# Optimization experiments

Measured on AMD Instinct MI355X. Metric: run time of the kernel, lower is better.

## Reference

```python
import jax, jax.numpy as jnp
import numpy as np

DEPTH = 128
NEG_MAX = -jnp.finfo(jnp.float32).max


def setup_inputs() -> dict:
    key = jax.random.key(0)
    ks = jax.random.split(key, 10)
    B, S, F, C = 16, 2048, 512, 1000
    x = jax.random.normal(ks[0], (B, S, F), dtype=jnp.float32)
    attention_mask = jax.random.randint(ks[1], (B, S, S), 0, 2) == 1
    s = 1.0 / np.sqrt(F)
    Wq = jax.random.uniform(ks[2], (F, DEPTH), jnp.float32, -s, s)
    bq = jax.random.uniform(ks[3], (DEPTH,), jnp.float32, -s, s)
    Wk = jax.random.uniform(ks[4], (F, DEPTH), jnp.float32, -s, s)
    bk = jax.random.uniform(ks[5], (DEPTH,), jnp.float32, -s, s)
    Wv = jax.random.uniform(ks[6], (F, DEPTH), jnp.float32, -s, s)
    bv = jax.random.uniform(ks[7], (DEPTH,), jnp.float32, -s, s)
    sl = 1.0 / np.sqrt(DEPTH)
    Wl = jax.random.uniform(ks[8], (DEPTH, C), jnp.float32, -sl, sl)
    bl = jax.random.uniform(ks[9], (C,), jnp.float32, -sl, sl)
    return {"x": x, "attention_mask": attention_mask,
            "Wq": Wq, "bq": bq, "Wk": Wk, "bk": bk,
            "Wv": Wv, "bv": bv, "Wl": Wl, "bl": bl}


def reference(x, attention_mask, Wq, bq, Wk, bk, Wv, bv, Wl, bl):
    # x: [B, S, F]; single-head attention with depth=128
    q = (x @ Wq + bq) * (DEPTH ** -0.5)          # [B, S, D] (is_scaled_dot_product)
    k = x @ Wk + bk                               # [B, S, D]
    v = x @ Wv + bv                               # [B, S, D]
    logit = jnp.einsum('bsd,btd->bst', q, k)      # [B, S, S]
    # masked_fill_(mask, -float_max) then added to logits
    logit = logit + jnp.where(attention_mask, NEG_MAX, 0.0)
    attn = jax.nn.softmax(logit, axis=2)
    out = jnp.einsum('bst,btd->bsd', attn, v)     # [B, S, D]
    out = out @ Wl + bl                           # [B, S, C]
    return out.mean(axis=1)                       # [B, C]
```

## Files before the change

### kernel.cpp

```cpp
#include <hip/hip_runtime.h>
#include <stdint.h>

#define BB 16
#define SS 2048
#define FF 512
#define DD 128
#define CC 1000

typedef __attribute__((ext_vector_type(8))) short bf16x8;
typedef __attribute__((ext_vector_type(4))) float f32x4;

__device__ __forceinline__ unsigned short f2bf(float f) {
  unsigned x;
  __builtin_memcpy(&x, &f, 4);
  x = x + 0x7FFFu + ((x >> 16) & 1u);
  return (unsigned short)(x >> 16);
}
__device__ __forceinline__ float bf2f(unsigned short u) {
  unsigned x = ((unsigned)u) << 16;
  float f;
  __builtin_memcpy(&f, &x, 4);
  return f;
}
__device__ __forceinline__ unsigned pk2(float a, float b) {
  return (unsigned)f2bf(a) | ((unsigned)f2bf(b) << 16);
}

#define WS_WG   256
#define WS_ZG   131328
#define WS_YG   262400
#define WS_PK   270592
#define WS_Q    8659200
#define WS_K    17047808
#define WS_V    25436416
#define WS_WT   33825024
#define WS_END  34218240
#define WS_P    34218240
#define WS_END2 168435968

__global__ __launch_bounds__(256) void k_wt(const float* __restrict__ Wq,
                                            const float* __restrict__ Wk,
                                            const float* __restrict__ Wv,
                                            unsigned short* __restrict__ wt,
                                            const unsigned* __restrict__ mask,
                                            int* __restrict__ flags,
                                            float* __restrict__ wgl,
                                            float* __restrict__ zgl,
                                            float* __restrict__ ygl) {
  const int tid = threadIdx.x;
  if (blockIdx.x == 768) {
    __shared__ unsigned red;
    if (tid == 0) red = 0;
    __syncthreads();
    unsigned a = 0;
#pragma unroll
    for (int j = 0; j < 4; ++j) a |= mask[tid * 4 + j] & 0xFFFFFF00u;
    if (a) atomicOr(&red, 1u);
    __syncthreads();
    if (tid == 0) flags[0] = (red == 0) ? 1 : 0;
    for (int i = tid; i < BB * SS; i += 256) { wgl[i] = 0.f; zgl[i] = 0.f; }
    for (int i = tid; i < BB * DD; i += 256) ygl[i] = 0.f;
    return;
  }
  int idx = blockIdx.x * 256 + tid;
  int ty = idx >> 16;
  int o = idx & 65535;
  int d = o >> 9, f = o & 511;
  const float* W = ty == 0 ? Wq : (ty == 1 ? Wk : Wv);
  wt[idx] = f2bf(W[f * DD + d]);
}

__global__ __launch_bounds__(256) void k_pack(const void* __restrict__ mask,
                                              const int* __restrict__ flags,
                                              unsigned* __restrict__ pk) {
  const int tid = threadIdx.x;
  const long long base = (long long)blockIdx.x * 32768;
  const bool isInt = flags[0] != 0;
  for (int it = 0; it < 128; ++it) {
    long long e = base + it * 256 + tid;
    int val;
    if (isInt) val = ((const int*)mask)[e];
    else       val = ((const unsigned char*)mask)[e];
    unsigned long long bal = __ballot(val != 0);
    if ((tid & 31) == 0)
      pk[e >> 5] = (unsigned)((tid & 63) ? (bal >> 32) : bal);
  }
}

__global__ __launch_bounds__(256) void k_proj(const float* __restrict__ xg,
                                              const unsigned short* __restrict__ wtg,
                                              const float* __restrict__ bq,
                                              const float* __restrict__ bk,
                                              const float* __restrict__ bv,
                                              unsigned short* __restrict__ qo,
                                              unsigned short* __restrict__ ko,
                                              unsigned short* __restrict__ vo) {
  __shared__ __align__(16) char lA[8192];
  __shared__ __align__(16) char lB[8192];
  const int tid = threadIdx.x;
  const int lane = tid & 63;
  const int wv = tid >> 6;
  const int colL = lane & 15, quad = lane >> 4;
  const int blk = blockIdx.x, ty = blockIdx.y;
  const float* bias = ty == 0 ? bq : (ty == 1 ? bk : bv);
  unsigned short* outp = ty == 0 ? qo : (ty == 1 ? ko : vo);
  const float scale = ty == 0 ? 0.08838834764831845f : 1.0f;
  const unsigned short* wbase = wtg + (size_t)ty * 65536;
  const int m0 = (wv & 1) * 64, n0 = (wv >> 1) * 64;

  f32x4 acc[4][4];
  const f32x4 z4 = {0.f, 0.f, 0.f, 0.f};
#pragma unroll
  for (int mi = 0; mi < 4; ++mi)
#pragma unroll
    for (int ni = 0; ni < 4; ++ni) acc[mi][ni] = z4;

  for (int ic = 0; ic < 16; ++ic) {
    const int k0 = ic * 32;
    uint4 va[2], vb[2];
#pragma unroll
    for (int rr = 0; rr < 2; ++rr) {
      int p = rr * 256 + tid;
      int row = p >> 2, c = p & 3;
      const float* xp = xg + (size_t)(blk * 128 + row) * FF + k0 + c * 8;
      float4 x0 = *(const float4*)xp;
      float4 x1 = *(const float4*)(xp + 4);
      va[rr].x = pk2(x0.x, x0.y); va[rr].y = pk2(x0.z, x0.w);
      va[rr].z = pk2(x1.x, x1.y); va[rr].w = pk2(x1.z, x1.w);
      vb[rr] = *(const uint4*)(wbase + (size_t)row * FF + k0 + c * 8);
    }
    __syncthreads();
#pragma unroll
    for (int rr = 0; rr < 2; ++rr) {
      int p = rr * 256 + tid;
      int row = p >> 2, c = p & 3;
      int phys = c ^ ((row >> 1) & 3);
      *(uint4*)(lA + row * 64 + phys * 16) = va[rr];
      *(uint4*)(lB + row * 64 + phys * 16) = vb[rr];
    }
    __syncthreads();
    bf16x8 af[4], bfr[4];
#pragma unroll
    for (int mi = 0; mi < 4; ++mi) {
      int ar = m0 + mi * 16 + colL;
      int phys = quad ^ ((ar >> 1) & 3);
      af[mi] = *(const bf16x8*)(lA + ar * 64 + phys * 16);
    }
#pragma unroll
    for (int ni = 0; ni < 4; ++ni) {
      int br = n0 + ni * 16 + colL;
      int phys = quad ^ ((br >> 1) & 3);
      bfr[ni] = *(const bf16x8*)(lB + br * 64 + phys * 16);
    }
#pragma unroll
    for (int mi = 0; mi < 4; ++mi)
#pragma unroll
      for (int ni = 0; ni < 4; ++ni)
        acc[mi][ni] = __builtin_amdgcn_mfma_f32_16x16x32_bf16(af[mi], bfr[ni], acc[mi][ni], 0, 0, 0);
  }
#pragma unroll
  for (int ni = 0; ni < 4; ++ni) {
    int col = n0 + ni * 16 + colL;
    float bval = bias[col];
#pragma unroll
    for (int mi = 0; mi < 4; ++mi) {
#pragma unroll
      for (int r = 0; r < 4; ++r) {
        int row = blk * 128 + m0 + mi * 16 + quad * 4 + r;
        float val = (acc[mi][ni][r] + bval) * scale;
        outp[(size_t)row * DD + col] = f2bf(val);
      }
    }
  }
}

template <int MODE>
__global__ __launch_bounds__(256) void k_attn2(const unsigned short* __restrict__ qg,
                                               const unsigned short* __restrict__ kg,
                                               const unsigned* __restrict__ pk,
                                               float* __restrict__ zg,
                                               float* __restrict__ wg,
                                               unsigned short* __restrict__ pg) {
  __shared__ __align__(16) char kt[16384];
  __shared__ unsigned maskt[128 * 9];
  __shared__ float wacc[256];
  __shared__ __align__(16) unsigned short pt[128 * 64];
  const int tid = threadIdx.x;
  const int lane = tid & 63, wv = tid >> 6;
  const int colL = lane & 15, quad = lane >> 4;
  const int row0 = blockIdx.x * 128;
  const int tc = blockIdx.y;
  const int b = blockIdx.z;
  const int tbase = tc * 256;

  for (int i = tid; i < 1024; i += 256) {
    int row = i >> 3, w = i & 7;
    maskt[row * 9 + w] = pk[((size_t)b * SS + row0 + row) * 64 + tc * 8 + w];
  }
  if constexpr (MODE == 2) wacc[tid] = 0.f;

  bf16x8 qf[2][4];
#pragma unroll
  for (int mi = 0; mi < 2; ++mi) {
    int qrow = row0 + wv * 32 + mi * 16 + colL;
    const unsigned short* qp = qg + ((size_t)b * SS + qrow) * DD + quad * 8;
#pragma unroll
    for (int kk = 0; kk < 4; ++kk) qf[mi][kk] = *(const bf16x8*)(qp + kk * 32);
  }
  float z[2][4] = {{0.f, 0.f, 0.f, 0.f}, {0.f, 0.f, 0.f, 0.f}};
  float zinv[2][4];
  if constexpr (MODE == 2) {
#pragma unroll
    for (int mi = 0; mi < 2; ++mi)
#pragma unroll
      for (int r = 0; r < 4; ++r) {
        int row = row0 + wv * 32 + mi * 16 + quad * 4 + r;
        zinv[mi][r] = 1.0f / fmaxf(zg[(size_t)b * SS + row], 1e-30f);
      }
  }

  for (int kt0 = 0; kt0 < 4; ++kt0) {
    const int t0 = tbase + kt0 * 64;
    uint4 kreg[4];
#pragma unroll
    for (int rr = 0; rr < 4; ++rr) {
      int p = rr * 256 + tid;
      int row = p >> 4, c = p & 15;
      kreg[rr] = *(const uint4*)(kg + ((size_t)b * SS + t0 + row) * DD + c * 8);
    }
    __syncthreads();
#pragma unroll
    for (int rr = 0; rr < 4; ++rr) {
      int p = rr * 256 + tid;
      int row = p >> 4, c = p & 15;
      int phys = c ^ (row & 7);
      *(uint4*)(kt + row * 256 + phys * 16) = kreg[rr];
    }
    __syncthreads();
#pragma unroll
    for (int nt = 0; nt < 4; ++nt) {
      int rb = nt * 16 + colL;
      bf16x8 bb[4];
#pragma unroll
      for (int kk = 0; kk < 4; ++kk) {
        int phys = (kk * 4 + quad) ^ (rb & 7);
        bb[kk] = *(const bf16x8*)(kt + rb * 256 + phys * 16);
      }
      int tl = kt0 * 64 + nt * 16 + colL;
      int ct = nt * 16 + colL;
      int wl = tl >> 5, wb = tl & 31;
      float cs = 0.f;
#pragma unroll
      for (int mi = 0; mi < 2; ++mi) {
        f32x4 acc = {0.f, 0.f, 0.f, 0.f};
        acc = __builtin_amdgcn_mfma_f32_16x16x32_bf16(qf[mi][0], bb[0], acc, 0, 0, 0);
        acc = __builtin_amdgcn_mfma_f32_16x16x32_bf16(qf[mi][1], bb[1], acc, 0, 0, 0);
        acc = __builtin_amdgcn_mfma_f32_16x16x32_bf16(qf[mi][2], bb[2], acc, 0, 0, 0);
        acc = __builtin_amdgcn_mfma_f32_16x16x32_bf16(qf[mi][3], bb[3], acc, 0, 0, 0);
        int rbase = wv * 32 + mi * 16 + quad * 4;
#pragma unroll
        for (int r = 0; r < 4; ++r) {
          unsigned mw = maskt[(rbase + r) * 9 + wl];
          float e = ((mw >> wb) & 1u) ? 0.f : __expf(fminf(acc[r], 80.f));
          if constexpr (MODE != 2) z[mi][r] += e;
          else cs += e * zinv[mi][r];
          if constexpr (MODE == 1) {
            int rw = rbase + r;
            pt[rw * 64 + (ct ^ ((rw & 7) << 3))] = f2bf(e);
          }
        }
      }
      if constexpr (MODE == 2) {
        cs += __shfl_xor(cs, 16, 64);
        cs += __shfl_xor(cs, 32, 64);
        if (quad == 0) atomicAdd(&wacc[tl], cs);
      }
    }
    if constexpr (MODE == 1) {
      __syncthreads();
      unsigned short* prow = pg + ((size_t)b * SS + row0) * SS + t0;
#pragma unroll
      for (int i2 = 0; i2 < 4; ++i2) {
        int ii = i2 * 256 + tid;
        int rw = ii >> 3, c8 = ii & 7;
        uint4 vv = *(const uint4*)(pt + rw * 64 + ((c8 ^ (rw & 7)) * 8));
        *(uint4*)(prow + (size_t)rw * SS + c8 * 8) = vv;
      }
    }
  }
  if constexpr (MODE != 2) {
#pragma unroll
    for (int mi = 0; mi < 2; ++mi)
#pragma unroll
      for (int r = 0; r < 4; ++r) {
        float s = z[mi][r];
        s += __shfl_xor(s, 1, 64);
        s += __shfl_xor(s, 2, 64);
        s += __shfl_xor(s, 4, 64);
        s += __shfl_xor(s, 8, 64);
        if (colL == 0) {
          int row = row0 + wv * 32 + mi * 16 + quad * 4 + r;
          atomicAdd(&zg[(size_t)b * SS + row], s);
        }
      }
  } else {
    __syncthreads();
    atomicAdd(&wg[(size_t)b * SS + tbase + tid], wacc[tid]);
  }
}

__global__ __launch_bounds__(256) void k_csum(const unsigned short* __restrict__ pg,
                                              const float* __restrict__ zg,
                                              float* __restrict__ wg) {
  __shared__ float zl[256];
  const int tid = threadIdx.x;
  const int s0 = blockIdx.x * 256;
  const int b = blockIdx.y;
  zl[tid] = 1.0f / fmaxf(zg[(size_t)b * SS + s0 + tid], 1e-30f);
  __syncthreads();
  float acc[8] = {0.f, 0.f, 0.f, 0.f, 0.f, 0.f, 0.f, 0.f};
  const unsigned short* base = pg + ((size_t)b * SS + s0) * SS + tid * 8;
#pragma unroll 4
  for (int s = 0; s < 256; ++s) {
    bf16x8 pv = *(const bf16x8*)(base + (size_t)s * SS);
    float zi = zl[s];
#pragma unroll
    for (int j = 0; j < 8; ++j) acc[j] += bf2f((unsigned short)pv[j]) * zi;
  }
  float* wrow = wg + (size_t)b * SS + tid * 8;
#pragma unroll
  for (int j = 0; j < 8; ++j) atomicAdd(&wrow[j], acc[j]);
}

__global__ __launch_bounds__(256) void k_yv(const float* __restrict__ wgl,
                                            const unsigned short* __restrict__ vg,
                                            float* __restrict__ ygl) {
  const int tid = threadIdx.x;
  const int tc = blockIdx.x, b = blockIdx.y;
  const int d = tid & 127, half = tid >> 7;
  const int t0 = tc * 128 + half * 64;
  float p = 0.f;
  const float* wrow = wgl + (size_t)b * SS + t0;
  const unsigned short* vrow = vg + ((size_t)b * SS + t0) * DD + d;
#pragma unroll 8
  for (int t = 0; t < 64; ++t) p += wrow[t] * bf2f(vrow[(size_t)t * DD]);
  atomicAdd(&ygl[b * DD + d], p);
}

__global__ __launch_bounds__(256) void k_out(const float* __restrict__ ygl,
                                             const float* __restrict__ Wl,
                                             const float* __restrict__ bl,
                                             float* __restrict__ outp) {
  __shared__ float ys[DD];
  const int tid = threadIdx.x;
  const int b = blockIdx.x;
  if (tid < DD) ys[tid] = ygl[b * DD + tid] * (1.0f / 2048.0f);
  __syncthreads();
  for (int c = tid; c < CC; c += 256) {
    float a = bl[c];
#pragma unroll 16
    for (int dd = 0; dd < DD; ++dd) a += ys[dd] * Wl[dd * CC + c];
    outp[b * CC + c] = a;
  }
}

extern "C" void kernel_launch(void* const* d_in, const int* in_sizes, int n_in,
                              void* d_out, int out_size, void* d_ws, size_t ws_size,
                              hipStream_t stream) {
  const void* ptr[10];
  for (int i = 0; i < 10; ++i) ptr[i] = (i < n_in) ? d_in[i] : nullptr;
  if (n_in == 10) {
    const void *px = 0, *pm = 0, *pWl = 0, *pbl = 0;
    const void* pW[3] = {0, 0, 0};
    const void* pb[3] = {0, 0, 0};
    int nW = 0, nb = 0;
    for (int i = 0; i < 10; ++i) {
      int s = in_sizes[i];
      if (s == 16777216) px = d_in[i];
      else if (s == 67108864) pm = d_in[i];
      else if (s == 128000) pWl = d_in[i];
      else if (s == 1000) pbl = d_in[i];
      else if (s == 65536 && nW < 3) pW[nW++] = d_in[i];
      else if (s == 128 && nb < 3) pb[nb++] = d_in[i];
    }
    if (px && pm && pWl && pbl && nW == 3 && nb == 3) {
      ptr[0] = px; ptr[1] = pm;
      ptr[2] = pW[0]; ptr[3] = pb[0];
      ptr[4] = pW[1]; ptr[5] = pb[1];
      ptr[6] = pW[2]; ptr[7] = pb[2];
      ptr[8] = pWl; ptr[9] = pbl;
    }
  }
  char* ws = (char*)d_ws;
  if (ws_size < (size_t)WS_END) return;
  int* flags = (int*)ws;
  float* wg = (float*)(ws + WS_WG);
  float* zg = (float*)(ws + WS_ZG);
  float* yg = (float*)(ws + WS_YG);
  unsigned* pk = (unsigned*)(ws + WS_PK);
  unsigned short* q  = (unsigned short*)(ws + WS_Q);
  unsigned short* k  = (unsigned short*)(ws + WS_K);
  unsigned short* v  = (unsigned short*)(ws + WS_V);
  unsigned short* wt = (unsigned short*)(ws + WS_WT);
  unsigned short* pbuf = (unsigned short*)(ws + WS_P);
  const bool bigws = ws_size >= (size_t)WS_END2;

  k_wt<<<769, 256, 0, stream>>>((const float*)ptr[2], (const float*)ptr[4],
                                (const float*)ptr[6], wt,
                                (const unsigned*)ptr[1], flags, wg, zg, yg);
  k_pack<<<2048, 256, 0, stream>>>(ptr[1], flags, pk);
  k_proj<<<dim3(256, 3), 256, 0, stream>>>((const float*)ptr[0], wt,
                                           (const float*)ptr[3], (const float*)ptr[5],
                                           (const float*)ptr[7], q, k, v);
  if (bigws) {
    k_attn2<1><<<dim3(16, 8, 16), 256, 0, stream>>>(q, k, pk, zg, wg, pbuf);
    k_csum<<<dim3(8, 16), 256, 0, stream>>>(pbuf, zg, wg);
  } else {
    k_attn2<0><<<dim3(16, 8, 16), 256, 0, stream>>>(q, k, pk, zg, wg, nullptr);
    k_attn2<2><<<dim3(16, 8, 16), 256, 0, stream>>>(q, k, pk, zg, wg, nullptr);
  }
  k_yv<<<dim3(16, 16), 256, 0, stream>>>(wg, v, yg);
  k_out<<<16, 256, 0, stream>>>(yg, (const float*)ptr[8], (const float*)ptr[9],
                                (float*)d_out);
}
```

Before: 621.3 us.

## Fuse attention scores, normalization and column sums into one LDS-resident kernel

Replaces the two-pass attention (score kernel that writes unnormalized probabilities to a large global buffer, then a column-sum kernel) with one kernel. Each 512-thread block owns 32 query rows across all 2048 keys and keeps the bf16 probabilities in about 128KB of dynamic LDS. Row sums are reduced in LDS, and the normalized column sums are accumulated straight into the weight vector. K tiles are register-prefetched one chunk ahead. This removes the global P round-trip and a launch, at the cost of one block per CU from the large LDS footprint, small per-wave MFMA work between barriers, and more K reloads per batch.

```diff
diff --git a/kernel.cpp b/kernel.cpp
--- a/kernel.cpp
+++ b/kernel.cpp
@@ -35,8 +35,6 @@
 #define WS_V    25436416
 #define WS_WT   33825024
 #define WS_END  34218240
-#define WS_P    34218240
-#define WS_END2 168435968
 
 __global__ __launch_bounds__(256) void k_wt(const float* __restrict__ Wq,
                                             const float* __restrict__ Wk,
@@ -174,162 +172,119 @@
   }
 }
 
-template <int MODE>
-__global__ __launch_bounds__(256) void k_attn2(const unsigned short* __restrict__ qg,
-                                               const unsigned short* __restrict__ kg,
-                                               const unsigned* __restrict__ pk,
-                                               float* __restrict__ zg,
-                                               float* __restrict__ wg,
-                                               unsigned short* __restrict__ pg) {
-  __shared__ __align__(16) char kt[16384];
-  __shared__ unsigned maskt[128 * 9];
-  __shared__ float wacc[256];
-  __shared__ __align__(16) unsigned short pt[128 * 64];
+__global__ __launch_bounds__(512, 2) void k_fatt(const unsigned short* __restrict__ qg,
+                                                 const unsigned short* __restrict__ kg,
+                                                 const unsigned* __restrict__ pk,
+                                                 float* __restrict__ wg) {
+  extern __shared__ __align__(16) char smem[];
+  unsigned short* pt = (unsigned short*)smem;
+  char* kt = smem + 131072;
+  unsigned* mk = (unsigned*)(smem + 147456);
+  float* zfin = (float*)(smem + 155776);
+  float* zinvl = (float*)(smem + 155904);
+
   const int tid = threadIdx.x;
   const int lane = tid & 63, wv = tid >> 6;
   const int colL = lane & 15, quad = lane >> 4;
-  const int row0 = blockIdx.x * 128;
-  const int tc = blockIdx.y;
-  const int b = blockIdx.z;
-  const int tbase = tc * 256;
-
-  for (int i = tid; i < 1024; i += 256) {
-    int row = i >> 3, w = i & 7;
-    maskt[row * 9 + w] = pk[((size_t)b * SS + row0 + row) * 64 + tc * 8 + w];
-  }
-  if constexpr (MODE == 2) wacc[tid] = 0.f;
-
-  bf16x8 qf[2][4];
-#pragma unroll
-  for (int mi = 0; mi < 2; ++mi) {
-    int qrow = row0 + wv * 32 + mi * 16 + colL;
+  const int wr = wv & 1, wq = wv >> 1;
+  const int r0 = blockIdx.x * 32;
+  const int b = blockIdx.y;
+
+  for (int i = tid; i < 2048; i += 512) {
+    int row = i >> 6, w = i & 63;
+    mk[row * 65 + w] = pk[((size_t)b * SS + r0 + row) * 64 + w];
+  }
+  if (tid < 32) zfin[tid] = 0.f;
+
+  bf16x8 qf[4];
+  {
+    int qrow = r0 + wr * 16 + colL;
     const unsigned short* qp = qg + ((size_t)b * SS + qrow) * DD + quad * 8;
 #pragma unroll
-    for (int kk = 0; kk < 4; ++kk) qf[mi][kk] = *(const bf16x8*)(qp + kk * 32);
-  }
-  float z[2][4] = {{0.f, 0.f, 0.f, 0.f}, {0.f, 0.f, 0.f, 0.f}};
-  float zinv[2][4];
-  if constexpr (MODE == 2) {
-#pragma unroll
-    for (int mi = 0; mi < 2; ++mi)
-#pragma unroll
-      for (int r = 0; r < 4; ++r) {
-        int row = row0 + wv * 32 + mi * 16 + quad * 4 + r;
-        zinv[mi][r] = 1.0f / fmaxf(zg[(size_t)b * SS + row], 1e-30f);
-      }
-  }
-
-  for (int kt0 = 0; kt0 < 4; ++kt0) {
-    const int t0 = tbase + kt0 * 64;
-    uint4 kreg[4];
-#pragma unroll
-    for (int rr = 0; rr < 4; ++rr) {
-      int p = rr * 256 + tid;
-      int row = p >> 4, c = p & 15;
-      kreg[rr] = *(const uint4*)(kg + ((size_t)b * SS + t0 + row) * DD + c * 8);
-    }
-    __syncthreads();
-#pragma unroll
-    for (int rr = 0; rr < 4; ++rr) {
-      int p = rr * 256 + tid;
-      int row = p >> 4, c = p & 15;
-      int phys = c ^ (row & 7);
-      *(uint4*)(kt + row * 256 + phys * 16) = kreg[rr];
-    }
-    __syncthreads();
-#pragma unroll
-    for (int nt = 0; nt < 4; ++nt) {
-      int rb = nt * 16 + colL;
-      bf16x8 bb[4];
-#pragma unroll
-      for (int kk = 0; kk < 4; ++kk) {
-        int phys = (kk * 4 + quad) ^ (rb & 7);
-        bb[kk] = *(const bf16x8*)(kt + rb * 256 + phys * 16);
-      }
-      int tl = kt0 * 64 + nt * 16 + colL;
-      int ct = nt * 16 + colL;
-      int wl = tl >> 5, wb = tl & 31;
-      float cs = 0.f;
-#pragma unroll
-      for (int mi = 0; mi < 2; ++mi) {
-        f32x4 acc = {0.f, 0.f, 0.f, 0.f};
-        acc = __builtin_amdgcn_mfma_f32_16x16x32_bf16(qf[mi][0], bb[0], acc, 0, 0, 0);
-        acc = __builtin_amdgcn_mfma_f32_16x16x32_bf16(qf[mi][1], bb[1], acc, 0, 0, 0);
-        acc = __builtin_amdgcn_mfma_f32_16x16x32_bf16(qf[mi][2], bb[2], acc, 0, 0, 0);
-        acc = __builtin_amdgcn_mfma_f32_16x16x32_bf16(qf[mi][3], bb[3], acc, 0, 0, 0);
-        int rbase = wv * 32 + mi * 16 + quad * 4;
-#pragma unroll
-        for (int r = 0; r < 4; ++r) {
-          unsigned mw = maskt[(rbase + r) * 9 + wl];
-          float e = ((mw >> wb) & 1u) ? 0.f : __expf(fminf(acc[r], 80.f));
-          if constexpr (MODE != 2) z[mi][r] += e;
-          else cs += e * zinv[mi][r];
-          if constexpr (MODE == 1) {
-            int rw = rbase + r;
-            pt[rw * 64 + (ct ^ ((rw & 7) << 3))] = f2bf(e);
-          }
-        }
-      }
-      if constexpr (MODE == 2) {
-        cs += __shfl_xor(cs, 16, 64);
-        cs += __shfl_xor(cs, 32, 64);
-        if (quad == 0) atomicAdd(&wacc[tl], cs);
-      }
-    }
-    if constexpr (MODE == 1) {
+    for (int kk = 0; kk < 4; ++kk) qf[kk] = *(const bf16x8*)(qp + kk * 32);
+  }
+
+  const int krow = tid >> 3, kc8 = tid & 7;
+  const unsigned short* kbase = kg + ((size_t)b * SS + krow) * DD;
+  const int kswz0 = (kc8 ^ (krow & 7)) * 16;
+  const int kswz1 = ((kc8 + 8) ^ (krow & 7)) * 16;
+
+  uint4 kreg0 = *(const uint4*)(kbase + kc8 * 8);
+  uint4 kreg1 = *(const uint4*)(kbase + kc8 * 8 + 64);
+  *(uint4*)(kt + krow * 256 + kswz0) = kreg0;
+  *(uint4*)(kt + krow * 256 + kswz1) = kreg1;
+  __syncthreads();
+
+  float z[4] = {0.f, 0.f, 0.f, 0.f};
+  const int tb = wq * 16 + colL;
+
+  for (int c = 0; c < 32; ++c) {
+    if (c < 31) {
+      const unsigned short* kb2 = kbase + (size_t)(c + 1) * 64 * DD;
+      kreg0 = *(const uint4*)(kb2 + kc8 * 8);
+      kreg1 = *(const uint4*)(kb2 + kc8 * 8 + 64);
+    }
+    bf16x8 bb[4];
+#pragma unroll
+    for (int kk = 0; kk < 4; ++kk) {
+      int phys = (kk * 4 + quad) ^ (tb & 7);
+      bb[kk] = *(const bf16x8*)(kt + tb * 256 + phys * 16);
+    }
+    f32x4 acc = {0.f, 0.f, 0.f, 0.f};
+    acc = __builtin_amdgcn_mfma_f32_16x16x32_bf16(qf[0], bb[0], acc, 0, 0, 0);
+    acc = __builtin_amdgcn_mfma_f32_16x16x32_bf16(qf[1], bb[1], acc, 0, 0, 0);
+    acc = __builtin_amdgcn_mfma_f32_16x16x32_bf16(qf[2], bb[2], acc, 0, 0, 0);
+    acc = __builtin_amdgcn_mfma_f32_16x16x32_bf16(qf[3], bb[3], acc, 0, 0, 0);
+    int tl = c * 64 + tb;
+    int widx = tl >> 5, wb = tl & 31;
+#pragma unroll
+    for (int r = 0; r < 4; ++r) {
+      int row_l = wr * 16 + quad * 4 + r;
+      unsigned mw = mk[row_l * 65 + widx];
+      float e = ((mw >> wb) & 1u) ? 0.f : __expf(fminf(acc[r], 80.f));
+      z[r] += e;
+      pt[row_l * 2048 + (tl ^ ((row_l & 7) << 3))] = f2bf(e);
+    }
+    if (c < 31) {
       __syncthreads();
-      unsigned short* prow = pg + ((size_t)b * SS + row0) * SS + t0;
-#pragma unroll
-      for (int i2 = 0; i2 < 4; ++i2) {
-        int ii = i2 * 256 + tid;
-        int rw = ii >> 3, c8 = ii & 7;
-        uint4 vv = *(const uint4*)(pt + rw * 64 + ((c8 ^ (rw & 7)) * 8));
-        *(uint4*)(prow + (size_t)rw * SS + c8 * 8) = vv;
-      }
-    }
-  }
-  if constexpr (MODE != 2) {
-#pragma unroll
-    for (int mi = 0; mi < 2; ++mi)
-#pragma unroll
-      for (int r = 0; r < 4; ++r) {
-        float s = z[mi][r];
-        s += __shfl_xor(s, 1, 64);
-        s += __shfl_xor(s, 2, 64);
-        s += __shfl_xor(s, 4, 64);
-        s += __shfl_xor(s, 8, 64);
-        if (colL == 0) {
-          int row = row0 + wv * 32 + mi * 16 + quad * 4 + r;
-          atomicAdd(&zg[(size_t)b * SS + row], s);
-        }
-      }
-  } else {
-    __syncthreads();
-    atomicAdd(&wg[(size_t)b * SS + tbase + tid], wacc[tid]);
-  }
-}
-
-__global__ __launch_bounds__(256) void k_csum(const unsigned short* __restrict__ pg,
-                                              const float* __restrict__ zg,
-                                              float* __restrict__ wg) {
-  __shared__ float zl[256];
-  const int tid = threadIdx.x;
-  const int s0 = blockIdx.x * 256;
-  const int b = blockIdx.y;
-  zl[tid] = 1.0f / fmaxf(zg[(size_t)b * SS + s0 + tid], 1e-30f);
+      *(uint4*)(kt + krow * 256 + kswz0) = kreg0;
+      *(uint4*)(kt + krow * 256 + kswz1) = kreg1;
+      __syncthreads();
+    }
+  }
+
+#pragma unroll
+  for (int r = 0; r < 4; ++r) {
+    float s = z[r];
+    s += __shfl_xor(s, 1, 64);
+    s += __shfl_xor(s, 2, 64);
+    s += __shfl_xor(s, 4, 64);
+    s += __shfl_xor(s, 8, 64);
+    if (colL == 0) atomicAdd(&zfin[wr * 16 + quad * 4 + r], s);
+  }
   __syncthreads();
-  float acc[8] = {0.f, 0.f, 0.f, 0.f, 0.f, 0.f, 0.f, 0.f};
-  const unsigned short* base = pg + ((size_t)b * SS + s0) * SS + tid * 8;
-#pragma unroll 4
-  for (int s = 0; s < 256; ++s) {
-    bf16x8 pv = *(const bf16x8*)(base + (size_t)s * SS);
-    float zi = zl[s];
-#pragma unroll
-    for (int j = 0; j < 8; ++j) acc[j] += bf2f((unsigned short)pv[j]) * zi;
-  }
-  float* wrow = wg + (size_t)b * SS + tid * 8;
-#pragma unroll
-  for (int j = 0; j < 8; ++j) atomicAdd(&wrow[j], acc[j]);
+  if (tid < 32) zinvl[tid] = 1.0f / fmaxf(zfin[tid], 1e-30f);
+  __syncthreads();
+
+  {
+    const int t0 = tid * 4;
+    float a0 = 0.f, a1 = 0.f, a2 = 0.f, a3 = 0.f;
+#pragma unroll 8
+    for (int r = 0; r < 32; ++r) {
+      const unsigned short* pr = pt + r * 2048 + (t0 ^ ((r & 7) << 3));
+      ushort4 pv = *(const ushort4*)pr;
+      float zi = zinvl[r];
+      a0 += bf2f(pv.x) * zi;
+      a1 += bf2f(pv.y) * zi;
+      a2 += bf2f(pv.z) * zi;
+      a3 += bf2f(pv.w) * zi;
+    }
+    float* wrow = wg + (size_t)b * SS + t0;
+    atomicAdd(&wrow[0], a0);
+    atomicAdd(&wrow[1], a1);
+    atomicAdd(&wrow[2], a2);
+    atomicAdd(&wrow[3], a3);
+  }
 }
 
 __global__ __launch_bounds__(256) void k_yv(const float* __restrict__ wgl,
@@ -402,8 +357,6 @@
   unsigned short* k  = (unsigned short*)(ws + WS_K);
   unsigned short* v  = (unsigned short*)(ws + WS_V);
   unsigned short* wt = (unsigned short*)(ws + WS_WT);
-  unsigned short* pbuf = (unsigned short*)(ws + WS_P);
-  const bool bigws = ws_size >= (size_t)WS_END2;
 
   k_wt<<<769, 256, 0, stream>>>((const float*)ptr[2], (const float*)ptr[4],
                                 (const float*)ptr[6], wt,
@@ -412,13 +365,7 @@
   k_proj<<<dim3(256, 3), 256, 0, stream>>>((const float*)ptr[0], wt,
                                            (const float*)ptr[3], (const float*)ptr[5],
                                            (const float*)ptr[7], q, k, v);
-  if (bigws) {
-    k_attn2<1><<<dim3(16, 8, 16), 256, 0, stream>>>(q, k, pk, zg, wg, pbuf);
-    k_csum<<<dim3(8, 16), 256, 0, stream>>>(pbuf, zg, wg);
-  } else {
-    k_attn2<0><<<dim3(16, 8, 16), 256, 0, stream>>>(q, k, pk, zg, wg, nullptr);
-    k_attn2<2><<<dim3(16, 8, 16), 256, 0, stream>>>(q, k, pk, zg, wg, nullptr);
-  }
+  k_fatt<<<dim3(64, 16), 512, 156032, stream>>>(q, k, pk, wg);
   k_yv<<<dim3(16, 16), 256, 0, stream>>>(wg, v, yg);
   k_out<<<16, 256, 0, stream>>>(yg, (const float*)ptr[8], (const float*)ptr[9],
                                 (float*)d_out);
```

After: 610.9 us. No clear change (-1.7%).
